# Kernel tuning notes

Hardware: AMD Instinct MI355X
Metric: run time of the kernel (lower is better)

The kernel has to match this reference:

```python
import jax, jax.numpy as jnp
import numpy as np

EMBED_DIM = 1024
NUM_HEADS = 16
HEAD_DIM = EMBED_DIM // NUM_HEADS
R = 8
ALPHA = 32
SCALING = ALPHA / R


def setup_inputs() -> dict:
    key = jax.random.key(0)
    ks = jax.random.split(key, 12)
    d = EMBED_DIM
    s = 1.0 / np.sqrt(d)
    inp = {
        "x": jax.random.normal(ks[0], (4, 2048, d), dtype=jnp.float32),
        # base linear weights (torch layout: [out, in]) and biases
        "Wq": jax.random.normal(ks[1], (d, d), dtype=jnp.float32) * s,
        "bq": jax.random.normal(ks[2], (d,), dtype=jnp.float32) * s,
        "Wk": jax.random.normal(ks[3], (d, d), dtype=jnp.float32) * s,
        "bk": jax.random.normal(ks[4], (d,), dtype=jnp.float32) * s,
        "Wv": jax.random.normal(ks[5], (d, d), dtype=jnp.float32) * s,
        "bv": jax.random.normal(ks[6], (d,), dtype=jnp.float32) * s,
        "Wo": jax.random.normal(ks[7], (d, d), dtype=jnp.float32) * s,
        "bo": jax.random.normal(ks[8], (d,), dtype=jnp.float32) * s,
        # LoRA adapters for q and v: A [r, in], B [out, r]
        "Aq": jax.random.normal(ks[9], (R, d), dtype=jnp.float32) * s,
        "Bq": jnp.zeros((d, R), dtype=jnp.float32),
        "Av": jax.random.normal(ks[10], (R, d), dtype=jnp.float32) * s,
        "Bv": jnp.zeros((d, R), dtype=jnp.float32),
    }
    return inp


def _lora_linear(x, W, b, A, Bm):
    # base: x @ W.T + b ; lora: scaling * (x @ A.T) @ B.T
    return x @ W.T + b + SCALING * ((x @ A.T) @ Bm.T)


def reference(x, Wq, bq, Wk, bk, Wv, bv, Wo, bo, Aq, Bq, Av, Bv):
    B, T, C = x.shape
    H, D = NUM_HEADS, HEAD_DIM
    q = _lora_linear(x, Wq, bq, Aq, Bq)
    k = x @ Wk.T + bk
    v = _lora_linear(x, Wv, bv, Av, Bv)
    # [B, T, C] -> [B, H, T, D]
    q = q.reshape(B, T, H, D).transpose(0, 2, 1, 3)
    k = k.reshape(B, T, H, D).transpose(0, 2, 1, 3)
    v = v.reshape(B, T, H, D).transpose(0, 2, 1, 3)
    scores = jnp.einsum("bhqd,bhkd->bhqk", q, k) / np.sqrt(D).astype(np.float32)
    weights = jax.nn.softmax(scores, axis=-1)
    out = jnp.einsum("bhqk,bhkd->bhqd", weights, v)
    out = out.transpose(0, 2, 1, 3).reshape(B, T, C)
    return out @ Wo.T + bo
```

## Files before the change

kernel.cpp:

```cpp
#include <hip/hip_runtime.h>
#include <hip/hip_bf16.h>
#include <stdint.h>

namespace {
constexpr int kB = 4, kT = 2048, kC = 1024, kH = 16, kD = 64;
constexpr int kM = kB * kT;
constexpr int kR = 8;
constexpr float kScaling = 4.0f;
constexpr float kInvSqrtD = 0.125f;
}

typedef short short8 __attribute__((ext_vector_type(8)));
typedef float f32x4 __attribute__((ext_vector_type(4)));
typedef unsigned short ushort4v __attribute__((ext_vector_type(4)));
typedef unsigned short ushort8v __attribute__((ext_vector_type(8)));

__device__ inline uint32_t f32_to_bf16_rne(float f) {
  uint32_t u = __float_as_uint(f);
  return (u + 0x7fffu + ((u >> 16) & 1u)) >> 16;
}

__device__ inline void split4(const float4 v, ushort4v& h, ushort4v& l) {
  const float f[4] = {v.x, v.y, v.z, v.w};
#pragma unroll
  for (int j = 0; j < 4; ++j) {
    const uint32_t hb = f32_to_bf16_rne(f[j]);
    const float hf = __uint_as_float(hb << 16);
    const uint32_t lb = f32_to_bf16_rne(f[j] - hf);
    h[j] = (unsigned short)hb;
    l[j] = (unsigned short)lb;
  }
}

__global__ __launch_bounds__(256) void lora_xa_kernel(
    const float* __restrict__ x, const float* __restrict__ Aq,
    const float* __restrict__ Av, float* __restrict__ xa) {
  const int wave = threadIdx.x >> 6;
  const int lane = threadIdx.x & 63;
  const int row = (blockIdx.x << 2) + wave;
  const float4* xr = reinterpret_cast<const float4*>(x) + (size_t)row * (kC / 4);
  const float4* aq = reinterpret_cast<const float4*>(Aq);
  const float4* av = reinterpret_cast<const float4*>(Av);
  float acc[16];
#pragma unroll
  for (int r = 0; r < 16; ++r) acc[r] = 0.f;
#pragma unroll
  for (int jj = 0; jj < (kC / 4) / 64; ++jj) {
    const int j = lane + jj * 64;
    const float4 xv = xr[j];
#pragma unroll
    for (int r = 0; r < 8; ++r) {
      const float4 a = aq[r * (kC / 4) + j];
      acc[r] += xv.x * a.x + xv.y * a.y + xv.z * a.z + xv.w * a.w;
      const float4 b = av[r * (kC / 4) + j];
      acc[8 + r] += xv.x * b.x + xv.y * b.y + xv.z * b.z + xv.w * b.w;
    }
  }
#pragma unroll
  for (int r = 0; r < 16; ++r) {
    float v = acc[r];
#pragma unroll
    for (int off = 32; off > 0; off >>= 1) v += __shfl_xor(v, off, 64);
    if (lane == 0) xa[(size_t)row * 16 + r] = v;
  }
}

__global__ __launch_bounds__(256, 2) void gemm_bf16x3_kernel(
    const float* __restrict__ X, const float* __restrict__ W,
    const float* __restrict__ bias, const float* __restrict__ xa,
    const float* __restrict__ Bm, float* __restrict__ out,
    const int lora_sel ,
    const int out_bhtd) {
  constexpr int BK = 32;
  constexpr int LDP = 40;
  __shared__ unsigned short Ah[128 * LDP];
  __shared__ unsigned short Al[128 * LDP];
  __shared__ unsigned short Bh[128 * LDP];
  __shared__ unsigned short Bl[128 * LDP];

  const int tid = threadIdx.x;
  const int m0 = blockIdx.y << 7;
  const int n0 = blockIdx.x << 7;
  const int wave = tid >> 6, lane = tid & 63;
  const int wr = wave >> 1, wc = wave & 1;
  const int lrow = lane & 15;
  const int lkg = lane >> 4;

  const int r0 = tid >> 3;
  const int c4 = (tid & 7) << 2;
  const float* xbase = X + (size_t)(m0 + r0) * kC + c4;
  const float* wbase = W + (size_t)(n0 + r0) * kC + c4;

  f32x4 acc[4][4];
#pragma unroll
  for (int a = 0; a < 4; ++a)
#pragma unroll
    for (int b = 0; b < 4; ++b) acc[a][b] = (f32x4){0.f, 0.f, 0.f, 0.f};

  float4 ga[4], gb[4];
#pragma unroll
  for (int i = 0; i < 4; ++i) {
    ga[i] = *reinterpret_cast<const float4*>(xbase + (size_t)i * 32 * kC);
    gb[i] = *reinterpret_cast<const float4*>(wbase + (size_t)i * 32 * kC);
  }

  for (int k0 = 0; k0 < kC; k0 += BK) {
#pragma unroll
    for (int i = 0; i < 4; ++i) {
      const int ro = (r0 + 32 * i) * LDP + c4;
      ushort4v ha, la2, hb, lb;
      split4(ga[i], ha, la2);
      split4(gb[i], hb, lb);
      *reinterpret_cast<ushort4v*>(&Ah[ro]) = ha;
      *reinterpret_cast<ushort4v*>(&Al[ro]) = la2;
      *reinterpret_cast<ushort4v*>(&Bh[ro]) = hb;
      *reinterpret_cast<ushort4v*>(&Bl[ro]) = lb;
    }
    __syncthreads();

    if (k0 + BK < kC) {
#pragma unroll
      for (int i = 0; i < 4; ++i) {
        ga[i] = *reinterpret_cast<const float4*>(xbase + (k0 + BK) + (size_t)i * 32 * kC);
        gb[i] = *reinterpret_cast<const float4*>(wbase + (k0 + BK) + (size_t)i * 32 * kC);
      }
    }

    short8 ah[4], al[4];
#pragma unroll
    for (int rb = 0; rb < 4; ++rb) {
      const int off = (wr * 64 + rb * 16 + lrow) * LDP + lkg * 8;
      ah[rb] = *reinterpret_cast<const short8*>(&Ah[off]);
      al[rb] = *reinterpret_cast<const short8*>(&Al[off]);
    }
#pragma unroll
    for (int cb = 0; cb < 4; ++cb) {
      const int off = (wc * 64 + cb * 16 + lrow) * LDP + lkg * 8;
      const short8 bhf = *reinterpret_cast<const short8*>(&Bh[off]);
      const short8 blf = *reinterpret_cast<const short8*>(&Bl[off]);
#pragma unroll
      for (int rb = 0; rb < 4; ++rb) {
        acc[rb][cb] = __builtin_amdgcn_mfma_f32_16x16x32_bf16(ah[rb], bhf, acc[rb][cb], 0, 0, 0);
        acc[rb][cb] = __builtin_amdgcn_mfma_f32_16x16x32_bf16(ah[rb], blf, acc[rb][cb], 0, 0, 0);
        acc[rb][cb] = __builtin_amdgcn_mfma_f32_16x16x32_bf16(al[rb], bhf, acc[rb][cb], 0, 0, 0);
      }
    }
    __syncthreads();
  }

#pragma unroll
  for (int rb = 0; rb < 4; ++rb) {
#pragma unroll
    for (int i = 0; i < 4; ++i) {
      const int m = m0 + wr * 64 + rb * 16 + (lkg << 2) + i;
      float la[kR];
      if (lora_sel >= 0) {
#pragma unroll
        for (int r = 0; r < kR; ++r) la[r] = xa[(size_t)m * 16 + lora_sel + r];
      }
#pragma unroll
      for (int cb = 0; cb < 4; ++cb) {
        const int n = n0 + wc * 64 + cb * 16 + lrow;
        float v = acc[rb][cb][i] + bias[n];
        if (lora_sel >= 0) {
          float lv = 0.f;
#pragma unroll
          for (int r = 0; r < kR; ++r)
            lv = fmaf(la[r], Bm[(size_t)n * kR + r], lv);
          v += kScaling * lv;
        }
        if (out_bhtd) {
          const int bb_ = m >> 11;
          const int t = m & (kT - 1);
          const int h = n >> 6;
          const int dd = n & (kD - 1);
          out[(((size_t)bb_ * kH + h) * kT + t) * kD + dd] = v;
        } else {
          out[(size_t)m * kC + n] = v;
        }
      }
    }
  }
}

__global__ __launch_bounds__(256, 3) void attn_mfma_kernel(
    const float* __restrict__ q, const float* __restrict__ k,
    const float* __restrict__ v, float* __restrict__ ctx) {
  constexpr int LDP = 72;
  __shared__ unsigned short P0[64 * LDP];
  __shared__ unsigned short P1[64 * LDP];
  __shared__ unsigned short P2[64 * LDP];
  __shared__ unsigned short P3[64 * LDP];

  const int tid = threadIdx.x;
  const int wave = tid >> 6, lane = tid & 63;
  const int lrow = lane & 15, lg = lane >> 4;
  const int bh = blockIdx.y;
  const int q0 = blockIdx.x << 6;
  const int b = bh >> 4, h = bh & 15;
  const float* qp = q + (size_t)bh * kT * kD;
  const float* kp = k + (size_t)bh * kT * kD;
  const float* vp = v + (size_t)bh * kT * kD;

  const int sr = tid >> 2;
  const int scb = (tid & 3) << 2;

#pragma unroll
  for (int u = 0; u < 4; ++u) {
    const int c = scb + 16 * u;
    float4 t4 = *reinterpret_cast<const float4*>(qp + (size_t)(q0 + sr) * kD + c);
    t4.x *= kInvSqrtD; t4.y *= kInvSqrtD; t4.z *= kInvSqrtD; t4.w *= kInvSqrtD;
    ushort4v hh, ll;
    split4(t4, hh, ll);
    *reinterpret_cast<ushort4v*>(&P0[sr * LDP + c]) = hh;
    *reinterpret_cast<ushort4v*>(&P1[sr * LDP + c]) = ll;
  }
  __syncthreads();

  short8 qh[2], ql[2];
#pragma unroll
  for (int ds0 = 0; ds0 < 2; ++ds0) {
    const int off = (wave * 16 + lrow) * LDP + ds0 * 32 + lg * 8;
    qh[ds0] = *reinterpret_cast<const short8*>(&P0[off]);
    ql[ds0] = *reinterpret_cast<const short8*>(&P1[off]);
  }
  __syncthreads();

  f32x4 acc_o[4];
#pragma unroll
  for (int i = 0; i < 4; ++i) acc_o[i] = (f32x4){0.f, 0.f, 0.f, 0.f};
  float m_i = -3.0e38f, l_i = 0.f;

  for (int kt = 0; kt < kT / 64; ++kt) {
    const int k0 = kt << 6;
#pragma unroll
    for (int u = 0; u < 4; ++u) {
      const int c = scb + 16 * u;
      const float4 t4 = *reinterpret_cast<const float4*>(kp + (size_t)(k0 + sr) * kD + c);
      ushort4v hh, ll;
      split4(t4, hh, ll);
      *reinterpret_cast<ushort4v*>(&P0[sr * LDP + c]) = hh;
      *reinterpret_cast<ushort4v*>(&P1[sr * LDP + c]) = ll;
    }
    {
      const int vd = tid & 63;
      const int vk = wave << 4;
      unsigned short vbuf[16];
#pragma unroll
      for (int i = 0; i < 16; ++i)
        vbuf[i] = (unsigned short)f32_to_bf16_rne(vp[(size_t)(k0 + vk + i) * kD + vd]);
      ushort8v w0, w1;
#pragma unroll
      for (int i = 0; i < 8; ++i) { w0[i] = vbuf[i]; w1[i] = vbuf[8 + i]; }
      *reinterpret_cast<ushort8v*>(&P2[vd * LDP + vk]) = w0;
      *reinterpret_cast<ushort8v*>(&P2[vd * LDP + vk + 8]) = w1;
    }
    __syncthreads();

    f32x4 acc_s[4];
#pragma unroll
    for (int kvr = 0; kvr < 4; ++kvr) acc_s[kvr] = (f32x4){0.f, 0.f, 0.f, 0.f};
#pragma unroll
    for (int kvr = 0; kvr < 4; ++kvr) {
#pragma unroll
      for (int ds0 = 0; ds0 < 2; ++ds0) {
        const int off = (kvr * 16 + lrow) * LDP + ds0 * 32 + lg * 8;
        const short8 khf = *reinterpret_cast<const short8*>(&P0[off]);
        const short8 klf = *reinterpret_cast<const short8*>(&P1[off]);
        acc_s[kvr] = __builtin_amdgcn_mfma_f32_16x16x32_bf16(khf, qh[ds0], acc_s[kvr], 0, 0, 0);
        acc_s[kvr] = __builtin_amdgcn_mfma_f32_16x16x32_bf16(khf, ql[ds0], acc_s[kvr], 0, 0, 0);
        acc_s[kvr] = __builtin_amdgcn_mfma_f32_16x16x32_bf16(klf, qh[ds0], acc_s[kvr], 0, 0, 0);
      }
    }

    float mx = acc_s[0][0];
#pragma unroll
    for (int kvr = 0; kvr < 4; ++kvr)
#pragma unroll
      for (int i = 0; i < 4; ++i) mx = fmaxf(mx, acc_s[kvr][i]);
    mx = fmaxf(mx, __shfl_xor(mx, 16, 64));
    mx = fmaxf(mx, __shfl_xor(mx, 32, 64));
    const float mnew = fmaxf(m_i, mx);
    const float alpha = __expf(m_i - mnew);
    float rs = 0.f;
    float p[4][4];
#pragma unroll
    for (int kvr = 0; kvr < 4; ++kvr)
#pragma unroll
      for (int i = 0; i < 4; ++i) {
        p[kvr][i] = __expf(acc_s[kvr][i] - mnew);
        rs += p[kvr][i];
      }
    rs += __shfl_xor(rs, 16, 64);
    rs += __shfl_xor(rs, 32, 64);
    l_i = l_i * alpha + rs;
    m_i = mnew;
#pragma unroll
    for (int dr = 0; dr < 4; ++dr)
#pragma unroll
      for (int i = 0; i < 4; ++i) acc_o[dr][i] *= alpha;

#pragma unroll
    for (int kvr = 0; kvr < 4; ++kvr) {
      ushort4v pu;
#pragma unroll
      for (int i = 0; i < 4; ++i) pu[i] = (unsigned short)f32_to_bf16_rne(p[kvr][i]);
      *reinterpret_cast<ushort4v*>(&P3[(wave * 16 + lrow) * LDP + kvr * 16 + lg * 4]) = pu;
    }
    __builtin_amdgcn_sched_barrier(0);

#pragma unroll
    for (int ks = 0; ks < 2; ++ks) {
      const short8 pf = *reinterpret_cast<const short8*>(
          &P3[(wave * 16 + lrow) * LDP + ks * 32 + lg * 8]);
#pragma unroll
      for (int dr = 0; dr < 4; ++dr) {
        const short8 vf = *reinterpret_cast<const short8*>(
            &P2[(dr * 16 + lrow) * LDP + ks * 32 + lg * 8]);
        acc_o[dr] = __builtin_amdgcn_mfma_f32_16x16x32_bf16(vf, pf, acc_o[dr], 0, 0, 0);
      }
    }
    __syncthreads();
  }

  const float inv = 1.0f / l_i;
  const int qq = q0 + wave * 16 + lrow;
  float* op = ctx + ((size_t)b * kT + qq) * kC + (h << 6);
#pragma unroll
  for (int dr = 0; dr < 4; ++dr) {
    const float4 o4 = make_float4(acc_o[dr][0] * inv, acc_o[dr][1] * inv,
                                  acc_o[dr][2] * inv, acc_o[dr][3] * inv);
    *reinterpret_cast<float4*>(op + dr * 16 + lg * 4) = o4;
  }
}

extern "C" void kernel_launch(void* const* d_in, const int* in_sizes, int n_in,
                              void* d_out, int out_size, void* d_ws, size_t ws_size,
                              hipStream_t stream) {
  const float* x  = (const float*)d_in[0];
  const float* Wq = (const float*)d_in[1];
  const float* bq = (const float*)d_in[2];
  const float* Wk = (const float*)d_in[3];
  const float* bk = (const float*)d_in[4];
  const float* Wv = (const float*)d_in[5];
  const float* bv = (const float*)d_in[6];
  const float* Wo = (const float*)d_in[7];
  const float* bo = (const float*)d_in[8];
  const float* Aq = (const float*)d_in[9];
  const float* Bq = (const float*)d_in[10];
  const float* Av = (const float*)d_in[11];
  const float* Bv = (const float*)d_in[12];
  float* out = (float*)d_out;

  float* ws = (float*)d_ws;
  float* qb  = ws;
  float* kb  = qb  + (size_t)kM * kC;
  float* vb  = kb  + (size_t)kM * kC;
  float* ctx = vb  + (size_t)kM * kC;
  float* xa  = ctx + (size_t)kM * kC;

  hipLaunchKernelGGL(lora_xa_kernel, dim3(kM / 4), dim3(256), 0, stream,
                     x, Aq, Av, xa);

  const dim3 gg(kC / 128, kM / 128);
  hipLaunchKernelGGL(gemm_bf16x3_kernel, gg, dim3(256), 0, stream,
                     x, Wq, bq, xa, Bq, qb, 0, 1);
  hipLaunchKernelGGL(gemm_bf16x3_kernel, gg, dim3(256), 0, stream,
                     x, Wk, bk, nullptr, nullptr, kb, -1, 1);
  hipLaunchKernelGGL(gemm_bf16x3_kernel, gg, dim3(256), 0, stream,
                     x, Wv, bv, xa, Bv, vb, 8, 1);

  hipLaunchKernelGGL(attn_mfma_kernel, dim3(kT / 64, kB * kH), dim3(256), 0, stream,
                     qb, kb, vb, ctx);

  hipLaunchKernelGGL(gemm_bf16x3_kernel, gg, dim3(256), 0, stream,
                     ctx, Wo, bo, nullptr, nullptr, out, -1, 0);
}
```

Before: 671.6 us.

## Swizzle LDS layouts, pre-transpose V, and widen attention query tile

The GEMM shared-memory tiles become XOR-swizzled 128-byte rows that pack the hi and lo bf16 halves together, replacing the padded separate buffers to avoid LDS bank conflicts. The V projection now writes V transposed ([B,H,D,T]) with float4 stores, so attention can stage V^T with coalesced vector loads instead of strided scalar loads. The attention kernel processes 128 queries per block (32 per wave), loads Q directly into registers, and prefetches the next K/V tile into registers during compute. The cost is more LDS and registers per block and the removal of the 3-blocks-per-CU launch bound, which may lower occupancy.

```diff
diff --git a/kernel.cpp b/kernel.cpp
--- a/kernel.cpp
+++ b/kernel.cpp
@@ -30,6 +30,13 @@
     h[j] = (unsigned short)hb;
     l[j] = (unsigned short)lb;
   }
+}
+
+__device__ inline short8 pack8(ushort4v a, ushort4v b) {
+  short8 r;
+  r[0] = (short)a[0]; r[1] = (short)a[1]; r[2] = (short)a[2]; r[3] = (short)a[3];
+  r[4] = (short)b[0]; r[5] = (short)b[1]; r[6] = (short)b[2]; r[7] = (short)b[3];
+  return r;
 }
 
 __global__ __launch_bounds__(256) void lora_xa_kernel(
@@ -70,13 +77,10 @@
     const float* __restrict__ bias, const float* __restrict__ xa,
     const float* __restrict__ Bm, float* __restrict__ out,
     const int lora_sel ,
-    const int out_bhtd) {
+    const int out_mode) {
   constexpr int BK = 32;
-  constexpr int LDP = 40;
-  __shared__ unsigned short Ah[128 * LDP];
-  __shared__ unsigned short Al[128 * LDP];
-  __shared__ unsigned short Bh[128 * LDP];
-  __shared__ unsigned short Bl[128 * LDP];
+  __shared__ __align__(16) unsigned char sA[128 * 128];
+  __shared__ __align__(16) unsigned char sB[128 * 128];
 
   const int tid = threadIdx.x;
   const int m0 = blockIdx.y << 7;
@@ -90,6 +94,8 @@
   const int c4 = (tid & 7) << 2;
   const float* xbase = X + (size_t)(m0 + r0) * kC + c4;
   const float* wbase = W + (size_t)(n0 + r0) * kC + c4;
+  const int ch = c4 >> 3;
+  const int slot = (c4 & 7) << 1;
 
   f32x4 acc[4][4];
 #pragma unroll
@@ -107,14 +113,16 @@
   for (int k0 = 0; k0 < kC; k0 += BK) {
 #pragma unroll
     for (int i = 0; i < 4; ++i) {
-      const int ro = (r0 + 32 * i) * LDP + c4;
-      ushort4v ha, la2, hb, lb;
-      split4(ga[i], ha, la2);
-      split4(gb[i], hb, lb);
-      *reinterpret_cast<ushort4v*>(&Ah[ro]) = ha;
-      *reinterpret_cast<ushort4v*>(&Al[ro]) = la2;
-      *reinterpret_cast<ushort4v*>(&Bh[ro]) = hb;
-      *reinterpret_cast<ushort4v*>(&Bl[ro]) = lb;
+      const int r = r0 + 32 * i;
+      const int rbase = r * 128;
+      const int s7 = r & 7;
+      ushort4v ha, la, hb2, lb2;
+      split4(ga[i], ha, la);
+      split4(gb[i], hb2, lb2);
+      *reinterpret_cast<ushort4v*>(&sA[rbase + ((ch ^ s7) << 4) + slot]) = ha;
+      *reinterpret_cast<ushort4v*>(&sA[rbase + (((ch | 4) ^ s7) << 4) + slot]) = la;
+      *reinterpret_cast<ushort4v*>(&sB[rbase + ((ch ^ s7) << 4) + slot]) = hb2;
+      *reinterpret_cast<ushort4v*>(&sB[rbase + (((ch | 4) ^ s7) << 4) + slot]) = lb2;
     }
     __syncthreads();
 
@@ -129,15 +137,15 @@
     short8 ah[4], al[4];
 #pragma unroll
     for (int rb = 0; rb < 4; ++rb) {
-      const int off = (wr * 64 + rb * 16 + lrow) * LDP + lkg * 8;
-      ah[rb] = *reinterpret_cast<const short8*>(&Ah[off]);
-      al[rb] = *reinterpret_cast<const short8*>(&Al[off]);
+      const int rA = wr * 64 + rb * 16 + lrow;
+      ah[rb] = *reinterpret_cast<const short8*>(&sA[rA * 128 + ((lkg ^ (rA & 7)) << 4)]);
+      al[rb] = *reinterpret_cast<const short8*>(&sA[rA * 128 + (((lkg | 4) ^ (rA & 7)) << 4)]);
     }
 #pragma unroll
     for (int cb = 0; cb < 4; ++cb) {
-      const int off = (wc * 64 + cb * 16 + lrow) * LDP + lkg * 8;
-      const short8 bhf = *reinterpret_cast<const short8*>(&Bh[off]);
-      const short8 blf = *reinterpret_cast<const short8*>(&Bl[off]);
+      const int rB = wc * 64 + cb * 16 + lrow;
+      const short8 bhf = *reinterpret_cast<const short8*>(&sB[rB * 128 + ((lkg ^ (rB & 7)) << 4)]);
+      const short8 blf = *reinterpret_cast<const short8*>(&sB[rB * 128 + (((lkg | 4) ^ (rB & 7)) << 4)]);
 #pragma unroll
       for (int rb = 0; rb < 4; ++rb) {
         acc[rb][cb] = __builtin_amdgcn_mfma_f32_16x16x32_bf16(ah[rb], bhf, acc[rb][cb], 0, 0, 0);
@@ -150,187 +158,240 @@
 
 #pragma unroll
   for (int rb = 0; rb < 4; ++rb) {
-#pragma unroll
-    for (int i = 0; i < 4; ++i) {
-      const int m = m0 + wr * 64 + rb * 16 + (lkg << 2) + i;
-      float la[kR];
-      if (lora_sel >= 0) {
-#pragma unroll
-        for (int r = 0; r < kR; ++r) la[r] = xa[(size_t)m * 16 + lora_sel + r];
-      }
-#pragma unroll
-      for (int cb = 0; cb < 4; ++cb) {
-        const int n = n0 + wc * 64 + cb * 16 + lrow;
-        float v = acc[rb][cb][i] + bias[n];
+    const int mbase = m0 + wr * 64 + rb * 16 + (lkg << 2);
+    float la2[4][kR];
+    if (lora_sel >= 0) {
+#pragma unroll
+      for (int i = 0; i < 4; ++i)
+#pragma unroll
+        for (int r = 0; r < kR; ++r)
+          la2[i][r] = xa[(size_t)(mbase + i) * 16 + lora_sel + r];
+    }
+#pragma unroll
+    for (int cb = 0; cb < 4; ++cb) {
+      const int n = n0 + wc * 64 + cb * 16 + lrow;
+      const float bi = bias[n];
+      float vv[4];
+#pragma unroll
+      for (int i = 0; i < 4; ++i) {
+        vv[i] = acc[rb][cb][i] + bi;
         if (lora_sel >= 0) {
           float lv = 0.f;
 #pragma unroll
           for (int r = 0; r < kR; ++r)
-            lv = fmaf(la[r], Bm[(size_t)n * kR + r], lv);
-          v += kScaling * lv;
+            lv = fmaf(la2[i][r], Bm[(size_t)n * kR + r], lv);
+          vv[i] += kScaling * lv;
         }
-        if (out_bhtd) {
+      }
+      if (out_mode == 2) {
+        const int bb_ = mbase >> 11;
+        const int t0 = mbase & (kT - 1);
+        const int hh = n >> 6;
+        const int dd = n & (kD - 1);
+        *reinterpret_cast<float4*>(
+            out + (((size_t)bb_ * kH + hh) * kD + dd) * kT + t0) =
+            make_float4(vv[0], vv[1], vv[2], vv[3]);
+      } else if (out_mode == 1) {
+#pragma unroll
+        for (int i = 0; i < 4; ++i) {
+          const int m = mbase + i;
           const int bb_ = m >> 11;
           const int t = m & (kT - 1);
-          const int h = n >> 6;
+          const int hh = n >> 6;
           const int dd = n & (kD - 1);
-          out[(((size_t)bb_ * kH + h) * kT + t) * kD + dd] = v;
-        } else {
-          out[(size_t)m * kC + n] = v;
+          out[(((size_t)bb_ * kH + hh) * kT + t) * kD + dd] = vv[i];
         }
-      }
-    }
-  }
-}
-
-__global__ __launch_bounds__(256, 3) void attn_mfma_kernel(
+      } else {
+#pragma unroll
+        for (int i = 0; i < 4; ++i)
+          out[(size_t)(mbase + i) * kC + n] = vv[i];
+      }
+    }
+  }
+}
+
+__global__ __launch_bounds__(256) void attn_mfma_kernel(
     const float* __restrict__ q, const float* __restrict__ k,
-    const float* __restrict__ v, float* __restrict__ ctx) {
-  constexpr int LDP = 72;
-  __shared__ unsigned short P0[64 * LDP];
-  __shared__ unsigned short P1[64 * LDP];
-  __shared__ unsigned short P2[64 * LDP];
-  __shared__ unsigned short P3[64 * LDP];
+    const float* __restrict__ vT, float* __restrict__ ctx) {
+  __shared__ __align__(16) unsigned char sKh[64 * 128];
+  __shared__ __align__(16) unsigned char sKl[64 * 128];
+  __shared__ __align__(16) unsigned char sVt[64 * 128];
+  __shared__ __align__(16) unsigned char sP[128 * 128];
 
   const int tid = threadIdx.x;
   const int wave = tid >> 6, lane = tid & 63;
   const int lrow = lane & 15, lg = lane >> 4;
   const int bh = blockIdx.y;
-  const int q0 = blockIdx.x << 6;
+  const int q0 = blockIdx.x << 7;
   const int b = bh >> 4, h = bh & 15;
-  const float* qp = q + (size_t)bh * kT * kD;
-  const float* kp = k + (size_t)bh * kT * kD;
-  const float* vp = v + (size_t)bh * kT * kD;
-
-  const int sr = tid >> 2;
-  const int scb = (tid & 3) << 2;
-
-#pragma unroll
-  for (int u = 0; u < 4; ++u) {
-    const int c = scb + 16 * u;
-    float4 t4 = *reinterpret_cast<const float4*>(qp + (size_t)(q0 + sr) * kD + c);
-    t4.x *= kInvSqrtD; t4.y *= kInvSqrtD; t4.z *= kInvSqrtD; t4.w *= kInvSqrtD;
-    ushort4v hh, ll;
-    split4(t4, hh, ll);
-    *reinterpret_cast<ushort4v*>(&P0[sr * LDP + c]) = hh;
-    *reinterpret_cast<ushort4v*>(&P1[sr * LDP + c]) = ll;
-  }
-  __syncthreads();
-
-  short8 qh[2], ql[2];
-#pragma unroll
-  for (int ds0 = 0; ds0 < 2; ++ds0) {
-    const int off = (wave * 16 + lrow) * LDP + ds0 * 32 + lg * 8;
-    qh[ds0] = *reinterpret_cast<const short8*>(&P0[off]);
-    ql[ds0] = *reinterpret_cast<const short8*>(&P1[off]);
-  }
-  __syncthreads();
-
-  f32x4 acc_o[4];
-#pragma unroll
-  for (int i = 0; i < 4; ++i) acc_o[i] = (f32x4){0.f, 0.f, 0.f, 0.f};
-  float m_i = -3.0e38f, l_i = 0.f;
-
-  for (int kt = 0; kt < kT / 64; ++kt) {
-    const int k0 = kt << 6;
-#pragma unroll
-    for (int u = 0; u < 4; ++u) {
-      const int c = scb + 16 * u;
-      const float4 t4 = *reinterpret_cast<const float4*>(kp + (size_t)(k0 + sr) * kD + c);
-      ushort4v hh, ll;
-      split4(t4, hh, ll);
-      *reinterpret_cast<ushort4v*>(&P0[sr * LDP + c]) = hh;
-      *reinterpret_cast<ushort4v*>(&P1[sr * LDP + c]) = ll;
-    }
+
+  const float* qbh = q + (size_t)bh * kT * kD;
+  const float* kbh = k + (size_t)bh * kT * kD;
+
+  const int srow = tid >> 2;
+  const int scq = (tid & 3) << 4;
+  const float* kstage = kbh + (size_t)srow * kD + scq;
+  const float* vstage = vT + ((size_t)bh * kD + srow) * kT + scq;
+
+  short8 qh[2][2], ql[2][2];
+#pragma unroll
+  for (int qs = 0; qs < 2; ++qs)
+#pragma unroll
+    for (int d0 = 0; d0 < 2; ++d0) {
+      const int qrow = q0 + wave * 32 + qs * 16 + lrow;
+      const float* qp2 = qbh + (size_t)qrow * kD + d0 * 32 + lg * 8;
+      float4 f0 = *reinterpret_cast<const float4*>(qp2);
+      float4 f1 = *reinterpret_cast<const float4*>(qp2 + 4);
+      f0.x *= kInvSqrtD; f0.y *= kInvSqrtD; f0.z *= kInvSqrtD; f0.w *= kInvSqrtD;
+      f1.x *= kInvSqrtD; f1.y *= kInvSqrtD; f1.z *= kInvSqrtD; f1.w *= kInvSqrtD;
+      ushort4v h0, l0, h1, l1;
+      split4(f0, h0, l0);
+      split4(f1, h1, l1);
+      qh[qs][d0] = pack8(h0, h1);
+      ql[qs][d0] = pack8(l0, l1);
+    }
+
+  f32x4 acc_o[2][4];
+#pragma unroll
+  for (int qs = 0; qs < 2; ++qs)
+#pragma unroll
+    for (int dr = 0; dr < 4; ++dr) acc_o[qs][dr] = (f32x4){0.f, 0.f, 0.f, 0.f};
+  float m_i[2] = {-3.0e38f, -3.0e38f};
+  float l_i[2] = {0.f, 0.f};
+
+  constexpr int kNT = kT / 64;
+  float4 kpre[4], vpre[4];
+#pragma unroll
+  for (int i = 0; i < 4; ++i) {
+    kpre[i] = *reinterpret_cast<const float4*>(kstage + i * 4);
+    vpre[i] = *reinterpret_cast<const float4*>(vstage + i * 4);
+  }
+
+  for (int kt = 0; kt < kNT; ++kt) {
     {
-      const int vd = tid & 63;
-      const int vk = wave << 4;
-      unsigned short vbuf[16];
-#pragma unroll
-      for (int i = 0; i < 16; ++i)
-        vbuf[i] = (unsigned short)f32_to_bf16_rne(vp[(size_t)(k0 + vk + i) * kD + vd]);
-      ushort8v w0, w1;
-#pragma unroll
-      for (int i = 0; i < 8; ++i) { w0[i] = vbuf[i]; w1[i] = vbuf[8 + i]; }
-      *reinterpret_cast<ushort8v*>(&P2[vd * LDP + vk]) = w0;
-      *reinterpret_cast<ushort8v*>(&P2[vd * LDP + vk + 8]) = w1;
+      const int s7k = srow & 7;
+#pragma unroll
+      for (int half = 0; half < 2; ++half) {
+        ushort4v h0, l0, h1, l1;
+        split4(kpre[2 * half], h0, l0);
+        split4(kpre[2 * half + 1], h1, l1);
+        const int chk = ((scq >> 3) + half) ^ s7k;
+        *reinterpret_cast<ushort8v*>(&sKh[srow * 128 + (chk << 4)]) =
+            (ushort8v){h0[0], h0[1], h0[2], h0[3], h1[0], h1[1], h1[2], h1[3]};
+        *reinterpret_cast<ushort8v*>(&sKl[srow * 128 + (chk << 4)]) =
+            (ushort8v){l0[0], l0[1], l0[2], l0[3], l1[0], l1[1], l1[2], l1[3]};
+        ushort8v w;
+        const float vf0[8] = {vpre[2 * half].x, vpre[2 * half].y,
+                              vpre[2 * half].z, vpre[2 * half].w,
+                              vpre[2 * half + 1].x, vpre[2 * half + 1].y,
+                              vpre[2 * half + 1].z, vpre[2 * half + 1].w};
+#pragma unroll
+        for (int e = 0; e < 8; ++e) w[e] = (unsigned short)f32_to_bf16_rne(vf0[e]);
+        *reinterpret_cast<ushort8v*>(&sVt[srow * 128 + (chk << 4)]) = w;
+      }
     }
     __syncthreads();
 
-    f32x4 acc_s[4];
-#pragma unroll
-    for (int kvr = 0; kvr < 4; ++kvr) acc_s[kvr] = (f32x4){0.f, 0.f, 0.f, 0.f};
-#pragma unroll
-    for (int kvr = 0; kvr < 4; ++kvr) {
-#pragma unroll
-      for (int ds0 = 0; ds0 < 2; ++ds0) {
-        const int off = (kvr * 16 + lrow) * LDP + ds0 * 32 + lg * 8;
-        const short8 khf = *reinterpret_cast<const short8*>(&P0[off]);
-        const short8 klf = *reinterpret_cast<const short8*>(&P1[off]);
-        acc_s[kvr] = __builtin_amdgcn_mfma_f32_16x16x32_bf16(khf, qh[ds0], acc_s[kvr], 0, 0, 0);
-        acc_s[kvr] = __builtin_amdgcn_mfma_f32_16x16x32_bf16(khf, ql[ds0], acc_s[kvr], 0, 0, 0);
-        acc_s[kvr] = __builtin_amdgcn_mfma_f32_16x16x32_bf16(klf, qh[ds0], acc_s[kvr], 0, 0, 0);
-      }
-    }
-
-    float mx = acc_s[0][0];
-#pragma unroll
-    for (int kvr = 0; kvr < 4; ++kvr)
-#pragma unroll
-      for (int i = 0; i < 4; ++i) mx = fmaxf(mx, acc_s[kvr][i]);
-    mx = fmaxf(mx, __shfl_xor(mx, 16, 64));
-    mx = fmaxf(mx, __shfl_xor(mx, 32, 64));
-    const float mnew = fmaxf(m_i, mx);
-    const float alpha = __expf(m_i - mnew);
-    float rs = 0.f;
-    float p[4][4];
-#pragma unroll
-    for (int kvr = 0; kvr < 4; ++kvr)
+    if (kt + 1 < kNT) {
+      const int knext = (kt + 1) << 6;
 #pragma unroll
       for (int i = 0; i < 4; ++i) {
-        p[kvr][i] = __expf(acc_s[kvr][i] - mnew);
-        rs += p[kvr][i];
-      }
-    rs += __shfl_xor(rs, 16, 64);
-    rs += __shfl_xor(rs, 32, 64);
-    l_i = l_i * alpha + rs;
-    m_i = mnew;
-#pragma unroll
-    for (int dr = 0; dr < 4; ++dr)
-#pragma unroll
-      for (int i = 0; i < 4; ++i) acc_o[dr][i] *= alpha;
-
-#pragma unroll
-    for (int kvr = 0; kvr < 4; ++kvr) {
-      ushort4v pu;
-#pragma unroll
-      for (int i = 0; i < 4; ++i) pu[i] = (unsigned short)f32_to_bf16_rne(p[kvr][i]);
-      *reinterpret_cast<ushort4v*>(&P3[(wave * 16 + lrow) * LDP + kvr * 16 + lg * 4]) = pu;
+        kpre[i] = *reinterpret_cast<const float4*>(kstage + (size_t)knext * kD + i * 4);
+        vpre[i] = *reinterpret_cast<const float4*>(vstage + knext + i * 4);
+      }
+    }
+
+    f32x4 acc_s[2][4];
+#pragma unroll
+    for (int qs = 0; qs < 2; ++qs)
+#pragma unroll
+      for (int kvr = 0; kvr < 4; ++kvr) acc_s[qs][kvr] = (f32x4){0.f, 0.f, 0.f, 0.f};
+#pragma unroll
+    for (int d0 = 0; d0 < 2; ++d0) {
+#pragma unroll
+      for (int kvr = 0; kvr < 4; ++kvr) {
+        const int rk = kvr * 16 + lrow;
+        const int byt = rk * 128 + ((((d0 << 2) + lg) ^ (rk & 7)) << 4);
+        const short8 khf = *reinterpret_cast<const short8*>(&sKh[byt]);
+        const short8 klf = *reinterpret_cast<const short8*>(&sKl[byt]);
+#pragma unroll
+        for (int qs = 0; qs < 2; ++qs) {
+          acc_s[qs][kvr] = __builtin_amdgcn_mfma_f32_16x16x32_bf16(khf, qh[qs][d0], acc_s[qs][kvr], 0, 0, 0);
+          acc_s[qs][kvr] = __builtin_amdgcn_mfma_f32_16x16x32_bf16(khf, ql[qs][d0], acc_s[qs][kvr], 0, 0, 0);
+          acc_s[qs][kvr] = __builtin_amdgcn_mfma_f32_16x16x32_bf16(klf, qh[qs][d0], acc_s[qs][kvr], 0, 0, 0);
+        }
+      }
+    }
+
+#pragma unroll
+    for (int qs = 0; qs < 2; ++qs) {
+      float mx = acc_s[qs][0][0];
+#pragma unroll
+      for (int kvr = 0; kvr < 4; ++kvr)
+#pragma unroll
+        for (int i = 0; i < 4; ++i) mx = fmaxf(mx, acc_s[qs][kvr][i]);
+      mx = fmaxf(mx, __shfl_xor(mx, 16, 64));
+      mx = fmaxf(mx, __shfl_xor(mx, 32, 64));
+      const float mnew = fmaxf(m_i[qs], mx);
+      const float alpha = __expf(m_i[qs] - mnew);
+      m_i[qs] = mnew;
+      const int prow = wave * 32 + qs * 16 + lrow;
+      const int p7 = prow & 7;
+      float rs = 0.f;
+#pragma unroll
+      for (int kvr = 0; kvr < 4; ++kvr) {
+        ushort4v pu;
+#pragma unroll
+        for (int i = 0; i < 4; ++i) {
+          const float pv = __expf(acc_s[qs][kvr][i] - mnew);
+          rs += pv;
+          pu[i] = (unsigned short)f32_to_bf16_rne(pv);
+        }
+        const int chunk = ((kvr << 1) + (lg >> 1)) ^ p7;
+        *reinterpret_cast<ushort4v*>(&sP[prow * 128 + (chunk << 4) + ((lg & 1) << 3)]) = pu;
+      }
+      rs += __shfl_xor(rs, 16, 64);
+      rs += __shfl_xor(rs, 32, 64);
+      l_i[qs] = l_i[qs] * alpha + rs;
+#pragma unroll
+      for (int dr = 0; dr < 4; ++dr)
+#pragma unroll
+        for (int i = 0; i < 4; ++i) acc_o[qs][dr][i] *= alpha;
     }
     __builtin_amdgcn_sched_barrier(0);
 
 #pragma unroll
     for (int ks = 0; ks < 2; ++ks) {
-      const short8 pf = *reinterpret_cast<const short8*>(
-          &P3[(wave * 16 + lrow) * LDP + ks * 32 + lg * 8]);
+      short8 pf[2];
+#pragma unroll
+      for (int qs = 0; qs < 2; ++qs) {
+        const int prow = wave * 32 + qs * 16 + lrow;
+        pf[qs] = *reinterpret_cast<const short8*>(
+            &sP[prow * 128 + ((((ks << 2) + lg) ^ (prow & 7)) << 4)]);
+      }
 #pragma unroll
       for (int dr = 0; dr < 4; ++dr) {
+        const int rv = dr * 16 + lrow;
         const short8 vf = *reinterpret_cast<const short8*>(
-            &P2[(dr * 16 + lrow) * LDP + ks * 32 + lg * 8]);
-        acc_o[dr] = __builtin_amdgcn_mfma_f32_16x16x32_bf16(vf, pf, acc_o[dr], 0, 0, 0);
+            &sVt[rv * 128 + ((((ks << 2) + lg) ^ (rv & 7)) << 4)]);
+        acc_o[0][dr] = __builtin_amdgcn_mfma_f32_16x16x32_bf16(vf, pf[0], acc_o[0][dr], 0, 0, 0);
+        acc_o[1][dr] = __builtin_amdgcn_mfma_f32_16x16x32_bf16(vf, pf[1], acc_o[1][dr], 0, 0, 0);
       }
     }
     __syncthreads();
   }
 
-  const float inv = 1.0f / l_i;
-  const int qq = q0 + wave * 16 + lrow;
-  float* op = ctx + ((size_t)b * kT + qq) * kC + (h << 6);
-#pragma unroll
-  for (int dr = 0; dr < 4; ++dr) {
-    const float4 o4 = make_float4(acc_o[dr][0] * inv, acc_o[dr][1] * inv,
-                                  acc_o[dr][2] * inv, acc_o[dr][3] * inv);
-    *reinterpret_cast<float4*>(op + dr * 16 + lg * 4) = o4;
+#pragma unroll
+  for (int qs = 0; qs < 2; ++qs) {
+    const float inv = 1.0f / l_i[qs];
+    const int qq = q0 + wave * 32 + qs * 16 + lrow;
+    float* op = ctx + ((size_t)b * kT + qq) * kC + (h << 6);
+#pragma unroll
+    for (int dr = 0; dr < 4; ++dr) {
+      const float4 o4 = make_float4(acc_o[qs][dr][0] * inv, acc_o[qs][dr][1] * inv,
+                                    acc_o[qs][dr][2] * inv, acc_o[qs][dr][3] * inv);
+      *reinterpret_cast<float4*>(op + dr * 16 + (lg << 2)) = o4;
+    }
   }
 }
 
@@ -355,8 +416,8 @@
   float* ws = (float*)d_ws;
   float* qb  = ws;
   float* kb  = qb  + (size_t)kM * kC;
-  float* vb  = kb  + (size_t)kM * kC;
-  float* ctx = vb  + (size_t)kM * kC;
+  float* vbT = kb  + (size_t)kM * kC;
+  float* ctx = vbT + (size_t)kM * kC;
   float* xa  = ctx + (size_t)kM * kC;
 
   hipLaunchKernelGGL(lora_xa_kernel, dim3(kM / 4), dim3(256), 0, stream,
@@ -368,10 +429,10 @@
   hipLaunchKernelGGL(gemm_bf16x3_kernel, gg, dim3(256), 0, stream,
                      x, Wk, bk, nullptr, nullptr, kb, -1, 1);
   hipLaunchKernelGGL(gemm_bf16x3_kernel, gg, dim3(256), 0, stream,
-                     x, Wv, bv, xa, Bv, vb, 8, 1);
-
-  hipLaunchKernelGGL(attn_mfma_kernel, dim3(kT / 64, kB * kH), dim3(256), 0, stream,
-                     qb, kb, vb, ctx);
+                     x, Wv, bv, xa, Bv, vbT, 8, 2);
+
+  hipLaunchKernelGGL(attn_mfma_kernel, dim3(kT / 128, kB * kH), dim3(256), 0, stream,
+                     qb, kb, vbT, ctx);
 
   hipLaunchKernelGGL(gemm_bf16x3_kernel, gg, dim3(256), 0, stream,
                      ctx, Wo, bo, nullptr, nullptr, out, -1, 0);
```

Measured after the change: 641.1 us. 4.5% less time.
